# Kernel optimization log

Hardware: AMD Instinct MI355X
Metric: run time of the kernel (lower is better)

## Reference

```python
import jax, jax.numpy as jnp
import numpy as np
import math

B, S, D, H = 2, 2048, 1024, 16
DK = D // H


def setup_inputs() -> dict:
    key = jax.random.key(0)
    ks = jax.random.split(key, 12)
    scale = 1.0 / math.sqrt(D)
    inp = {
        "q": jax.random.normal(ks[0], (B, S, D), jnp.float32),
        "k": jax.random.normal(ks[1], (B, S, D), jnp.float32),
        "v": jax.random.normal(ks[2], (B, S, D), jnp.float32),
        # causal mask, broadcast over batch and heads; 0 entries are masked out
        "mask": jnp.tril(jnp.ones((S, S), jnp.int32))[None, None, :, :],
        "wq_w": jax.random.normal(ks[3], (D, D), jnp.float32) * scale,
        "wq_b": jax.random.normal(ks[4], (D,), jnp.float32) * 0.01,
        "wk_w": jax.random.normal(ks[5], (D, D), jnp.float32) * scale,
        "wk_b": jax.random.normal(ks[6], (D,), jnp.float32) * 0.01,
        "wv_w": jax.random.normal(ks[7], (D, D), jnp.float32) * scale,
        "wv_b": jax.random.normal(ks[8], (D,), jnp.float32) * 0.01,
        "wo_w": jax.random.normal(ks[9], (D, D), jnp.float32) * scale,
        "wo_b": jax.random.normal(ks[10], (D,), jnp.float32) * 0.01,
    }
    return inp


def _mha(q, k, v, mask, wq_w, wq_b, wk_w, wk_b, wv_w, wv_b, wo_w, wo_b):
    # nn.Linear: x @ W^T + b
    def split_heads(x):  # [B,S,D] -> [B,H,S,DK]
        return x.reshape(B, S, H, DK).transpose(0, 2, 1, 3)

    Q = split_heads(q @ wq_w.T + wq_b)
    K = split_heads(k @ wk_w.T + wk_b)
    V = split_heads(v @ wv_w.T + wv_b)

    scores = jnp.einsum("bhqd,bhkd->bhqk", Q, K) / math.sqrt(DK)  # [B,H,S,S]
    scores = jnp.where(mask == 0, jnp.float32(-1e9), scores)
    # NOTE: source uses softmax(dim=1) == over the HEADS axis; replicated faithfully.
    attn = jax.nn.softmax(scores, axis=1)
    out = jnp.einsum("bhqk,bhkd->bhqd", attn, V)  # [B,H,S,DK]
    out = out.transpose(0, 2, 1, 3).reshape(B, S, D)
    return out @ wo_w.T + wo_b


def reference(q, k, v, mask, wq_w, wq_b, wk_w, wk_b, wv_w, wv_b, wo_w, wo_b):
    return _mha(q, k, v, mask, wq_w, wq_b, wk_w, wk_b, wv_w, wv_b, wo_w, wo_b)
```

## Files before the change

kernel.cpp:

```cpp
#include <hip/hip_runtime.h>
#include <hip/hip_bf16.h>
#include <stdint.h>


#define BB 2
#define SS 2048
#define DD 1024
#define HH 16
#define DKK 64

typedef __attribute__((ext_vector_type(8))) short bf16x8;
typedef __attribute__((ext_vector_type(4))) float f32x4;

typedef __attribute__((address_space(3))) uint32_t lds32_t;
typedef __attribute__((address_space(1))) uint32_t g32_t;

__device__ __forceinline__ void async_cp16(void* lds, const void* g){
    __builtin_amdgcn_global_load_lds((const g32_t*)g, (lds32_t*)lds, 16, 0, 0);
}

__device__ __forceinline__ float bf_lo(uint32_t w){ return __uint_as_float(w << 16); }
__device__ __forceinline__ float bf_hi(uint32_t w){ return __uint_as_float(w & 0xffff0000u); }
__device__ __forceinline__ uint16_t f2bf(float f){
    uint32_t x = __float_as_uint(f);
    return (uint16_t)((x + 0x7fffu + ((x >> 16) & 1u)) >> 16);
}
__device__ __forceinline__ void u4tof8(uint4 u, float* f){
    f[0]=bf_lo(u.x); f[1]=bf_hi(u.x);
    f[2]=bf_lo(u.y); f[3]=bf_hi(u.y);
    f[4]=bf_lo(u.z); f[5]=bf_hi(u.z);
    f[6]=bf_lo(u.w); f[7]=bf_hi(u.w);
}
__device__ __forceinline__ uint4 pack8u(const float* f){
    uint4 r;
    r.x = (uint32_t)f2bf(f[0]) | ((uint32_t)f2bf(f[1]) << 16);
    r.y = (uint32_t)f2bf(f[2]) | ((uint32_t)f2bf(f[3]) << 16);
    r.z = (uint32_t)f2bf(f[4]) | ((uint32_t)f2bf(f[5]) << 16);
    r.w = (uint32_t)f2bf(f[6]) | ((uint32_t)f2bf(f[7]) << 16);
    return r;
}

__global__ __launch_bounds__(256) void cvt_all(
    const float* __restrict__ w0, const float* __restrict__ w1,
    const float* __restrict__ w2, const float* __restrict__ w3,
    const float* __restrict__ a0, const float* __restrict__ a1,
    const float* __restrict__ a2,
    uint16_t* __restrict__ dw0, uint16_t* __restrict__ dw1,
    uint16_t* __restrict__ dw2, uint16_t* __restrict__ dw3,
    uint16_t* __restrict__ da0, uint16_t* __restrict__ da1,
    uint16_t* __restrict__ da2)
{
    const int y = blockIdx.y;
    const float* s; uint16_t* d; int n4;
    switch (y) {
        case 0: s = w0; d = dw0; n4 = 262144; break;
        case 1: s = w1; d = dw1; n4 = 262144; break;
        case 2: s = w2; d = dw2; n4 = 262144; break;
        case 3: s = w3; d = dw3; n4 = 262144; break;
        case 4: s = a0; d = da0; n4 = 1048576; break;
        case 5: s = a1; d = da1; n4 = 1048576; break;
        default: s = a2; d = da2; n4 = 1048576; break;
    }
    int i = blockIdx.x * 256 + threadIdx.x;
    if (i >= n4) return;
    float4 v = ((const float4*)s)[i];
    uint32_t lo = (uint32_t)f2bf(v.x) | ((uint32_t)f2bf(v.y) << 16);
    uint32_t hi = (uint32_t)f2bf(v.z) | ((uint32_t)f2bf(v.w) << 16);
    ((uint2*)d)[i] = make_uint2(lo, hi);
}

template <int OMODE>
__global__ __launch_bounds__(256) void gemm_bt(
    const uint16_t* __restrict__ A, const uint16_t* __restrict__ W,
    const float* __restrict__ bias, void* __restrict__ Cout)
{
    __shared__ uint16_t As[128][32];
    __shared__ uint16_t Bs[128][32];

    const int t    = threadIdx.x;
    const int bm   = blockIdx.x * 128;
    const int bn   = blockIdx.y * 128;
    const int lane = t & 63;
    const int w    = t >> 6;
    const int wm   = (w >> 1) * 64;
    const int wn   = (w & 1) * 64;
    const int lm   = lane & 15;
    const int quad = lane >> 4;

    f32x4 acc[4][4] = {};

    const int lr = lane >> 2;
    const int lc = (lane & 3) * 8;

    for (int k0 = 0; k0 < DD; k0 += 32) {
#pragma unroll
        for (int i2 = 0; i2 < 2; ++i2) {
            const int i = w * 2 + i2;
            async_cp16(&As[16*i][0], &A[(size_t)(bm + 16*i + lr) * DD + k0 + lc]);
            async_cp16(&Bs[16*i][0], &W[(size_t)(bn + 16*i + lr) * DD + k0 + lc]);
        }
        __syncthreads();
        bf16x8 af[4], bf[4];
#pragma unroll
        for (int mt = 0; mt < 4; ++mt) af[mt] = *(const bf16x8*)&As[wm + 16*mt + lm][quad*8];
#pragma unroll
        for (int nt = 0; nt < 4; ++nt) bf[nt] = *(const bf16x8*)&Bs[wn + 16*nt + lm][quad*8];
#pragma unroll
        for (int mt = 0; mt < 4; ++mt)
#pragma unroll
            for (int nt = 0; nt < 4; ++nt)
                acc[mt][nt] = __builtin_amdgcn_mfma_f32_16x16x32_bf16(af[mt], bf[nt], acc[mt][nt], 0, 0, 0);
        __syncthreads();
    }

#pragma unroll
    for (int nt = 0; nt < 4; ++nt) {
        const int ng = bn + wn + 16*nt + lm;
        const float bv = bias[ng];
#pragma unroll
        for (int mt = 0; mt < 4; ++mt) {
            const int m0 = bm + wm + 16*mt + quad*4;
            if (OMODE == 1) {
                const int bb = m0 >> 11, s0 = m0 & (SS - 1);
                const int hh = ng >> 6,  dk = ng & 63;
                float v0 = acc[mt][nt][0] + bv, v1 = acc[mt][nt][1] + bv;
                float v2 = acc[mt][nt][2] + bv, v3 = acc[mt][nt][3] + bv;
                uint2 wv;
                wv.x = (uint32_t)f2bf(v0) | ((uint32_t)f2bf(v1) << 16);
                wv.y = (uint32_t)f2bf(v2) | ((uint32_t)f2bf(v3) << 16);
                *(uint2*)&((uint16_t*)Cout)[(((size_t)(bb*HH + hh))*DKK + dk)*SS + s0] = wv;
            } else {
#pragma unroll
                for (int r = 0; r < 4; ++r) {
                    const int m = m0 + r;
                    const float val = acc[mt][nt][r] + bv;
                    if (OMODE == 0) {
                        const int bb = m >> 11, s = m & (SS - 1);
                        const int hh = ng >> 6, dk = ng & 63;
                        ((uint16_t*)Cout)[(((size_t)(bb*HH + hh))*SS + s)*DKK + dk] = f2bf(val);
                    } else {
                        ((float*)Cout)[(size_t)m * DD + ng] = val;
                    }
                }
            }
        }
    }
}

__global__ __launch_bounds__(256) void suf_kernel(
    const uint16_t* __restrict__ Vt, float* __restrict__ Suf)
{
    const int bh = blockIdx.x;
    const int t  = threadIdx.x;
    const int d = t & 63, seg = t >> 6;
    __shared__ float cs[64][65];
    const uint16_t* row = Vt + ((size_t)bh * DKK + d) * SS;
    for (int cl = 0; cl < 16; ++cl) {
        const int c = seg * 16 + cl;
        float sum = 0.f;
#pragma unroll
        for (int j = 0; j < 4; ++j) {
            uint4 u = *(const uint4*)&row[c * 32 + j * 8];
            float f[8]; u4tof8(u, f);
            sum += ((f[0]+f[1])+(f[2]+f[3])) + ((f[4]+f[5])+(f[6]+f[7]));
        }
        cs[c][d] = sum;
    }
    __syncthreads();
    if (t < 64) {
        float run = 0.f;
        Suf[((size_t)bh * 65 + 64) * DKK + t] = 0.f;
        for (int c = 63; c >= 0; --c) {
            run += cs[c][t];
            Suf[((size_t)bh * 65 + c) * DKK + t] = run;
        }
    }
}

__global__ __launch_bounds__(1024) void attn_v4(
    const uint16_t* __restrict__ Qc, const uint16_t* __restrict__ Kc,
    const uint16_t* __restrict__ Vt, const float* __restrict__ Suf,
    uint16_t* __restrict__ AOp)
{
    __shared__ uint16_t E[2][16][32][40];
    __shared__ uint16_t Zr[32][40];

    const int x  = blockIdx.x;
    const int p  = x & 3;
    const int b  = (x >> 2) & 1;
    const int pr = x >> 3;
    const int tid  = threadIdx.x;
    const int h    = tid >> 6;
    const int lane = tid & 63;
    const int lm   = lane & 15;
    const int quad = lane >> 4;

    const uint16_t* Qh = Qc + ((size_t)(b*HH + h)) * SS * DKK;
    const uint16_t* Kh = Kc + ((size_t)(b*HH + h)) * SS * DKK;
    const uint16_t* Vh = Vt + ((size_t)(b*HH + h)) * DKK * SS;
    uint16_t* AOb = AOp + ((size_t)(p*BB + b)) * SS * DD;

    const int rq = tid >> 4;
    const int rk2 = tid & 15;

    int cc = 0;
#pragma unroll
    for (int tt = 0; tt < 2; ++tt) {
        const int tq = tt ? (63 - pr) : pr;
        const int q0 = tq * 32;

        bf16x8 qf[2][2];
#pragma unroll
        for (int qt = 0; qt < 2; ++qt)
#pragma unroll
            for (int kd = 0; kd < 2; ++kd)
                qf[qt][kd] = *(const bf16x8*)&Qh[(size_t)(q0 + 16*qt + lm)*DKK + kd*32 + quad*8];

        f32x4 oacc[2][4] = {};

        for (int c = p; c <= tq; c += 4, ++cc) {
            const int buf = cc & 1;
            const int k0 = c * 32;
            bf16x8 vf[4];
#pragma unroll
            for (int dt = 0; dt < 4; ++dt)
                vf[dt] = *(const bf16x8*)&Vh[(size_t)(16*dt + lm)*SS + k0 + quad*8];
            f32x4 sacc[2][2] = {};
#pragma unroll
            for (int kt = 0; kt < 2; ++kt) {
                bf16x8 kf0 = *(const bf16x8*)&Kh[(size_t)(k0 + 16*kt + lm)*DKK + quad*8];
                bf16x8 kf1 = *(const bf16x8*)&Kh[(size_t)(k0 + 16*kt + lm)*DKK + 32 + quad*8];
#pragma unroll
                for (int qt = 0; qt < 2; ++qt) {
                    sacc[kt][qt] = __builtin_amdgcn_mfma_f32_16x16x32_bf16(kf0, qf[qt][0], sacc[kt][qt], 0, 0, 0);
                    sacc[kt][qt] = __builtin_amdgcn_mfma_f32_16x16x32_bf16(kf1, qf[qt][1], sacc[kt][qt], 0, 0, 0);
                }
            }
#pragma unroll
            for (int kt = 0; kt < 2; ++kt)
#pragma unroll
                for (int qt = 0; qt < 2; ++qt) {
                    const int qg = q0 + 16*qt + lm;
                    uint16_t ev[4];
#pragma unroll
                    for (int r = 0; r < 4; ++r) {
                        const int kg = k0 + 16*kt + quad*4 + r;
                        ev[r] = f2bf((kg > qg) ? 1.0f : __expf(sacc[kt][qt][r] * 0.125f));
                    }
                    uint2 evw;
                    evw.x = (uint32_t)ev[0] | ((uint32_t)ev[1] << 16);
                    evw.y = (uint32_t)ev[2] | ((uint32_t)ev[3] << 16);
                    *(uint2*)&E[buf][h][16*qt + lm][16*kt + quad*4] = evw;
                }
            __syncthreads();
            if (tid < 512) {
                float z0 = 0.f, z1 = 0.f;
#pragma unroll
                for (int i = 0; i < 16; ++i) {
                    uint32_t wv2 = *(const uint32_t*)&E[buf][i][rq][rk2*2];
                    z0 += bf_lo(wv2); z1 += bf_hi(wv2);
                }
                *(uint32_t*)&Zr[rq][rk2*2] =
                    (uint32_t)f2bf(__fdividef(1.f, z0)) | ((uint32_t)f2bf(__fdividef(1.f, z1)) << 16);
            }
            __syncthreads();
#pragma unroll
            for (int qt = 0; qt < 2; ++qt) {
                uint4 eu = *(const uint4*)&E[buf][h][16*qt + lm][quad*8];
                uint4 zu = *(const uint4*)&Zr[16*qt + lm][quad*8];
                float ef[8], zf[8];
                u4tof8(eu, ef); u4tof8(zu, zf);
                float pf[8];
#pragma unroll
                for (int j = 0; j < 8; ++j) pf[j] = ef[j] * zf[j];
                uint4 pu = pack8u(pf);
                bf16x8 pa = *(bf16x8*)&pu;
#pragma unroll
                for (int dt = 0; dt < 4; ++dt)
                    oacc[qt][dt] = __builtin_amdgcn_mfma_f32_16x16x32_bf16(pa, vf[dt], oacc[qt][dt], 0, 0, 0);
            }
        }

        float corr[4] = {0.f, 0.f, 0.f, 0.f};
        if (p == 0) {
            const float* Sf = Suf + ((size_t)(b*HH + h) * 65 + (tq + 1)) * DKK;
#pragma unroll
            for (int dt = 0; dt < 4; ++dt) corr[dt] = 0.0625f * Sf[16*dt + lm];
        }
#pragma unroll
        for (int qt = 0; qt < 2; ++qt)
#pragma unroll
            for (int dt = 0; dt < 4; ++dt)
#pragma unroll
                for (int r = 0; r < 4; ++r) {
                    const int s = q0 + 16*qt + quad*4 + r;
                    AOb[(size_t)s * DD + h*DKK + 16*dt + lm] = f2bf(oacc[qt][dt][r] + corr[dt]);
                }
    }
}

__global__ __launch_bounds__(256) void reduce4(uint16_t* AOp)
{
    const size_t P1 = (size_t)BB * SS * DD;
    const int i = blockIdx.x * 256 + threadIdx.x;
    uint2 u0 = ((const uint2*)AOp)[i];
    uint2 u1 = ((const uint2*)(AOp + P1))[i];
    uint2 u2 = ((const uint2*)(AOp + 2*P1))[i];
    uint2 u3 = ((const uint2*)(AOp + 3*P1))[i];
    float r[4];
    r[0] = (bf_lo(u0.x) + bf_lo(u1.x)) + (bf_lo(u2.x) + bf_lo(u3.x));
    r[1] = (bf_hi(u0.x) + bf_hi(u1.x)) + (bf_hi(u2.x) + bf_hi(u3.x));
    r[2] = (bf_lo(u0.y) + bf_lo(u1.y)) + (bf_lo(u2.y) + bf_lo(u3.y));
    r[3] = (bf_hi(u0.y) + bf_hi(u1.y)) + (bf_hi(u2.y) + bf_hi(u3.y));
    uint2 wv;
    wv.x = (uint32_t)f2bf(r[0]) | ((uint32_t)f2bf(r[1]) << 16);
    wv.y = (uint32_t)f2bf(r[2]) | ((uint32_t)f2bf(r[3]) << 16);
    ((uint2*)AOp)[i] = wv;
}

extern "C" void kernel_launch(void* const* d_in, const int* in_sizes, int n_in,
                              void* d_out, int out_size, void* d_ws, size_t ws_size,
                              hipStream_t stream)
{
    const float* q    = (const float*)d_in[0];
    const float* k    = (const float*)d_in[1];
    const float* v    = (const float*)d_in[2];
    const float* wq_w = (const float*)d_in[4];
    const float* wq_b = (const float*)d_in[5];
    const float* wk_w = (const float*)d_in[6];
    const float* wk_b = (const float*)d_in[7];
    const float* wv_w = (const float*)d_in[8];
    const float* wv_b = (const float*)d_in[9];
    const float* wo_w = (const float*)d_in[10];
    const float* wo_b = (const float*)d_in[11];
    float* out = (float*)d_out;

    uint16_t* wsu = (uint16_t*)d_ws;
    const size_t M1 = (size_t)1 << 20;
    uint16_t* wcq = wsu + 0 * M1;
    uint16_t* wck = wsu + 1 * M1;
    uint16_t* wcv = wsu + 2 * M1;
    uint16_t* wco = wsu + 3 * M1;
    uint16_t* Qc  = wsu + 4 * M1;
    uint16_t* Kc  = wsu + 8 * M1;
    uint16_t* Vt  = wsu + 12 * M1;
    uint16_t* AOp = wsu + 16 * M1;
    uint16_t* xq  = wsu + 16 * M1;
    uint16_t* xk  = wsu + 20 * M1;
    uint16_t* xv  = wsu + 24 * M1;
    float*    Suf = (float*)wcq;

    cvt_all<<<dim3(4096, 7), 256, 0, stream>>>(
        wq_w, wk_w, wv_w, wo_w, q, k, v,
        wcq, wck, wcv, wco, xq, xk, xv);

    dim3 ggrid(32, 8);
    gemm_bt<0><<<ggrid, 256, 0, stream>>>(xq, wcq, wq_b, Qc);
    gemm_bt<0><<<ggrid, 256, 0, stream>>>(xk, wck, wk_b, Kc);
    gemm_bt<1><<<ggrid, 256, 0, stream>>>(xv, wcv, wv_b, Vt);

    suf_kernel<<<32, 256, 0, stream>>>(Vt, Suf);
    attn_v4<<<256, 1024, 0, stream>>>(Qc, Kc, Vt, Suf, AOp);

    reduce4<<<4096, 256, 0, stream>>>(AOp);
    gemm_bt<2><<<ggrid, 256, 0, stream>>>(AOp, wco, wo_b, out);
}
```

Baseline: 316.5 us.

## Switch to fp16 with packed math, merge QKV GEMMs, split attention blocks per query tile

All intermediate storage moves from bf16 to fp16, using packed RTZ converts and packed half multiplies in place of the manual bf16 rounding and unpacking. The three projection GEMMs become one launch with a z-dimension of three. The attention kernel now handles a single query tile per block over 512 blocks instead of two tiles over 256, and drops the double-buffered E array, which adds a barrier before each E write. The aim is to cut conversion ALU work and launch overhead and to expose more parallelism, at the cost of fp16 range and rounding risk and more imbalanced block lengths.

```diff
diff --git a/kernel.cpp b/kernel.cpp
--- a/kernel.cpp
+++ b/kernel.cpp
@@ -1,5 +1,4 @@
 #include <hip/hip_runtime.h>
-#include <hip/hip_bf16.h>
 #include <stdint.h>
 
 
@@ -9,7 +8,10 @@
 #define HH 16
 #define DKK 64
 
-typedef __attribute__((ext_vector_type(8))) short bf16x8;
+typedef _Float16 f16;
+typedef __attribute__((ext_vector_type(2))) _Float16 f16x2;
+typedef __attribute__((ext_vector_type(8))) _Float16 f16x8;
+typedef __attribute__((ext_vector_type(2))) __fp16 fp16x2_raw;
 typedef __attribute__((ext_vector_type(4))) float f32x4;
 
 typedef __attribute__((address_space(3))) uint32_t lds32_t;
@@ -19,25 +21,18 @@
     __builtin_amdgcn_global_load_lds((const g32_t*)g, (lds32_t*)lds, 16, 0, 0);
 }
 
-__device__ __forceinline__ float bf_lo(uint32_t w){ return __uint_as_float(w << 16); }
-__device__ __forceinline__ float bf_hi(uint32_t w){ return __uint_as_float(w & 0xffff0000u); }
-__device__ __forceinline__ uint16_t f2bf(float f){
-    uint32_t x = __float_as_uint(f);
-    return (uint16_t)((x + 0x7fffu + ((x >> 16) & 1u)) >> 16);
-}
-__device__ __forceinline__ void u4tof8(uint4 u, float* f){
-    f[0]=bf_lo(u.x); f[1]=bf_hi(u.x);
-    f[2]=bf_lo(u.y); f[3]=bf_hi(u.y);
-    f[4]=bf_lo(u.z); f[5]=bf_hi(u.z);
-    f[6]=bf_lo(u.w); f[7]=bf_hi(u.w);
-}
-__device__ __forceinline__ uint4 pack8u(const float* f){
-    uint4 r;
-    r.x = (uint32_t)f2bf(f[0]) | ((uint32_t)f2bf(f[1]) << 16);
-    r.y = (uint32_t)f2bf(f[2]) | ((uint32_t)f2bf(f[3]) << 16);
-    r.z = (uint32_t)f2bf(f[4]) | ((uint32_t)f2bf(f[5]) << 16);
-    r.w = (uint32_t)f2bf(f[6]) | ((uint32_t)f2bf(f[7]) << 16);
-    return r;
+union U32H { uint32_t u; f16x2 h; fp16x2_raw hr; };
+
+__device__ __forceinline__ uint32_t pk2(float a, float b){
+    U32H c; c.hr = __builtin_amdgcn_cvt_pkrtz(a, b); return c.u;
+}
+__device__ __forceinline__ float h_lo(uint32_t w){ U32H c; c.u = w; return (float)c.h[0]; }
+__device__ __forceinline__ float h_hi(uint32_t w){ U32H c; c.u = w; return (float)c.h[1]; }
+__device__ __forceinline__ uint32_t pkmul(uint32_t a, uint32_t b){
+    U32H x, y, r; x.u = a; y.u = b; r.h = x.h * y.h; return r.u;
+}
+__device__ __forceinline__ uint16_t f2h(float f){
+    union { f16 h; uint16_t u; } c; c.h = (f16)f; return c.u;
 }
 
 __global__ __launch_bounds__(256) void cvt_all(
@@ -64,19 +59,15 @@
     int i = blockIdx.x * 256 + threadIdx.x;
     if (i >= n4) return;
     float4 v = ((const float4*)s)[i];
-    uint32_t lo = (uint32_t)f2bf(v.x) | ((uint32_t)f2bf(v.y) << 16);
-    uint32_t hi = (uint32_t)f2bf(v.z) | ((uint32_t)f2bf(v.w) << 16);
-    ((uint2*)d)[i] = make_uint2(lo, hi);
+    ((uint2*)d)[i] = make_uint2(pk2(v.x, v.y), pk2(v.z, v.w));
 }
 
 template <int OMODE>
-__global__ __launch_bounds__(256) void gemm_bt(
+__device__ __forceinline__ void gemm_core(
+    uint16_t (*As)[32], uint16_t (*Bs)[32],
     const uint16_t* __restrict__ A, const uint16_t* __restrict__ W,
     const float* __restrict__ bias, void* __restrict__ Cout)
 {
-    __shared__ uint16_t As[128][32];
-    __shared__ uint16_t Bs[128][32];
-
     const int t    = threadIdx.x;
     const int bm   = blockIdx.x * 128;
     const int bn   = blockIdx.y * 128;
@@ -100,16 +91,16 @@
             async_cp16(&Bs[16*i][0], &W[(size_t)(bn + 16*i + lr) * DD + k0 + lc]);
         }
         __syncthreads();
-        bf16x8 af[4], bf[4];
-#pragma unroll
-        for (int mt = 0; mt < 4; ++mt) af[mt] = *(const bf16x8*)&As[wm + 16*mt + lm][quad*8];
-#pragma unroll
-        for (int nt = 0; nt < 4; ++nt) bf[nt] = *(const bf16x8*)&Bs[wn + 16*nt + lm][quad*8];
+        f16x8 a8[4], b8[4];
+#pragma unroll
+        for (int mt = 0; mt < 4; ++mt) a8[mt] = *(const f16x8*)&As[wm + 16*mt + lm][quad*8];
+#pragma unroll
+        for (int nt = 0; nt < 4; ++nt) b8[nt] = *(const f16x8*)&Bs[wn + 16*nt + lm][quad*8];
 #pragma unroll
         for (int mt = 0; mt < 4; ++mt)
 #pragma unroll
             for (int nt = 0; nt < 4; ++nt)
-                acc[mt][nt] = __builtin_amdgcn_mfma_f32_16x16x32_bf16(af[mt], bf[nt], acc[mt][nt], 0, 0, 0);
+                acc[mt][nt] = __builtin_amdgcn_mfma_f32_16x16x32_f16(a8[mt], b8[nt], acc[mt][nt], 0, 0, 0);
         __syncthreads();
     }
 
@@ -123,11 +114,9 @@
             if (OMODE == 1) {
                 const int bb = m0 >> 11, s0 = m0 & (SS - 1);
                 const int hh = ng >> 6,  dk = ng & 63;
-                float v0 = acc[mt][nt][0] + bv, v1 = acc[mt][nt][1] + bv;
-                float v2 = acc[mt][nt][2] + bv, v3 = acc[mt][nt][3] + bv;
                 uint2 wv;
-                wv.x = (uint32_t)f2bf(v0) | ((uint32_t)f2bf(v1) << 16);
-                wv.y = (uint32_t)f2bf(v2) | ((uint32_t)f2bf(v3) << 16);
+                wv.x = pk2(acc[mt][nt][0] + bv, acc[mt][nt][1] + bv);
+                wv.y = pk2(acc[mt][nt][2] + bv, acc[mt][nt][3] + bv);
                 *(uint2*)&((uint16_t*)Cout)[(((size_t)(bb*HH + hh))*DKK + dk)*SS + s0] = wv;
             } else {
 #pragma unroll
@@ -137,7 +126,7 @@
                     if (OMODE == 0) {
                         const int bb = m >> 11, s = m & (SS - 1);
                         const int hh = ng >> 6, dk = ng & 63;
-                        ((uint16_t*)Cout)[(((size_t)(bb*HH + hh))*SS + s)*DKK + dk] = f2bf(val);
+                        ((uint16_t*)Cout)[(((size_t)(bb*HH + hh))*SS + s)*DKK + dk] = f2h(val);
                     } else {
                         ((float*)Cout)[(size_t)m * DD + ng] = val;
                     }
@@ -145,6 +134,31 @@
             }
         }
     }
+}
+
+__global__ __launch_bounds__(256) void gemm_qkv(
+    const uint16_t* __restrict__ xq, const uint16_t* __restrict__ wq,
+    const float* __restrict__ bq, uint16_t* __restrict__ Qc,
+    const uint16_t* __restrict__ xk, const uint16_t* __restrict__ wk,
+    const float* __restrict__ bk, uint16_t* __restrict__ Kc,
+    const uint16_t* __restrict__ xv, const uint16_t* __restrict__ wv,
+    const float* __restrict__ bv, uint16_t* __restrict__ Vt)
+{
+    __shared__ __align__(16) uint16_t As[128][32];
+    __shared__ __align__(16) uint16_t Bs[128][32];
+    const int z = blockIdx.z;
+    if (z == 0)      gemm_core<0>(As, Bs, xq, wq, bq, Qc);
+    else if (z == 1) gemm_core<0>(As, Bs, xk, wk, bk, Kc);
+    else             gemm_core<1>(As, Bs, xv, wv, bv, Vt);
+}
+
+__global__ __launch_bounds__(256) void gemm_o(
+    const uint16_t* __restrict__ A, const uint16_t* __restrict__ W,
+    const float* __restrict__ bias, float* __restrict__ Cout)
+{
+    __shared__ __align__(16) uint16_t As[128][32];
+    __shared__ __align__(16) uint16_t Bs[128][32];
+    gemm_core<2>(As, Bs, A, W, bias, Cout);
 }
 
 __global__ __launch_bounds__(256) void suf_kernel(
@@ -159,10 +173,10 @@
         const int c = seg * 16 + cl;
         float sum = 0.f;
 #pragma unroll
-        for (int j = 0; j < 4; ++j) {
-            uint4 u = *(const uint4*)&row[c * 32 + j * 8];
-            float f[8]; u4tof8(u, f);
-            sum += ((f[0]+f[1])+(f[2]+f[3])) + ((f[4]+f[5])+(f[6]+f[7]));
+        for (int jj = 0; jj < 4; ++jj) {
+            uint4 u = *(const uint4*)&row[c * 32 + jj * 8];
+            sum += ((h_lo(u.x)+h_hi(u.x)) + (h_lo(u.y)+h_hi(u.y)))
+                 + ((h_lo(u.z)+h_hi(u.z)) + (h_lo(u.w)+h_hi(u.w)));
         }
         cs[c][d] = sum;
     }
@@ -177,18 +191,19 @@
     }
 }
 
-__global__ __launch_bounds__(1024) void attn_v4(
+__global__ __launch_bounds__(1024, 8) void attn_v5(
     const uint16_t* __restrict__ Qc, const uint16_t* __restrict__ Kc,
     const uint16_t* __restrict__ Vt, const float* __restrict__ Suf,
     uint16_t* __restrict__ AOp)
 {
-    __shared__ uint16_t E[2][16][32][40];
-    __shared__ uint16_t Zr[32][40];
+    __shared__ __align__(16) uint16_t E[16][32][40];
+    __shared__ __align__(16) uint16_t Zr[32][40];
 
     const int x  = blockIdx.x;
     const int p  = x & 3;
     const int b  = (x >> 2) & 1;
-    const int pr = x >> 3;
+    const int j  = x >> 3;
+    const int tq = (j < 32) ? j : 95 - j;
     const int tid  = threadIdx.x;
     const int h    = tid >> 6;
     const int lane = tid & 63;
@@ -200,103 +215,91 @@
     const uint16_t* Vh = Vt + ((size_t)(b*HH + h)) * DKK * SS;
     uint16_t* AOb = AOp + ((size_t)(p*BB + b)) * SS * DD;
 
-    const int rq = tid >> 4;
+    const int rq  = tid >> 4;
     const int rk2 = tid & 15;
 
-    int cc = 0;
-#pragma unroll
-    for (int tt = 0; tt < 2; ++tt) {
-        const int tq = tt ? (63 - pr) : pr;
-        const int q0 = tq * 32;
-
-        bf16x8 qf[2][2];
-#pragma unroll
-        for (int qt = 0; qt < 2; ++qt)
-#pragma unroll
-            for (int kd = 0; kd < 2; ++kd)
-                qf[qt][kd] = *(const bf16x8*)&Qh[(size_t)(q0 + 16*qt + lm)*DKK + kd*32 + quad*8];
-
-        f32x4 oacc[2][4] = {};
-
-        for (int c = p; c <= tq; c += 4, ++cc) {
-            const int buf = cc & 1;
-            const int k0 = c * 32;
-            bf16x8 vf[4];
+    const int q0 = tq * 32;
+
+    f16x8 qf[2][2];
+#pragma unroll
+    for (int qt = 0; qt < 2; ++qt)
+#pragma unroll
+        for (int kd = 0; kd < 2; ++kd)
+            qf[qt][kd] = *(const f16x8*)&Qh[(size_t)(q0 + 16*qt + lm)*DKK + kd*32 + quad*8];
+
+    f32x4 oacc[2][4] = {};
+
+    for (int c = p; c <= tq; c += 4) {
+        const int k0 = c * 32;
+        f16x8 vf[4];
+#pragma unroll
+        for (int dt = 0; dt < 4; ++dt)
+            vf[dt] = *(const f16x8*)&Vh[(size_t)(16*dt + lm)*SS + k0 + quad*8];
+        f32x4 sacc[2][2] = {};
+#pragma unroll
+        for (int kt = 0; kt < 2; ++kt) {
+            f16x8 kf0 = *(const f16x8*)&Kh[(size_t)(k0 + 16*kt + lm)*DKK + quad*8];
+            f16x8 kf1 = *(const f16x8*)&Kh[(size_t)(k0 + 16*kt + lm)*DKK + 32 + quad*8];
+#pragma unroll
+            for (int qt = 0; qt < 2; ++qt) {
+                sacc[kt][qt] = __builtin_amdgcn_mfma_f32_16x16x32_f16(kf0, qf[qt][0], sacc[kt][qt], 0, 0, 0);
+                sacc[kt][qt] = __builtin_amdgcn_mfma_f32_16x16x32_f16(kf1, qf[qt][1], sacc[kt][qt], 0, 0, 0);
+            }
+        }
+        __syncthreads();
+#pragma unroll
+        for (int kt = 0; kt < 2; ++kt)
+#pragma unroll
+            for (int qt = 0; qt < 2; ++qt) {
+                const int qg = q0 + 16*qt + lm;
+                float e[4];
+#pragma unroll
+                for (int r = 0; r < 4; ++r) {
+                    const int kg = k0 + 16*kt + quad*4 + r;
+                    e[r] = (kg > qg) ? 1.0f : __expf(sacc[kt][qt][r] * 0.125f);
+                }
+                uint2 evw = make_uint2(pk2(e[0], e[1]), pk2(e[2], e[3]));
+                *(uint2*)&E[h][16*qt + lm][16*kt + quad*4] = evw;
+            }
+        __syncthreads();
+        if (tid < 512) {
+            float z0 = 0.f, z1 = 0.f;
+#pragma unroll
+            for (int i = 0; i < 16; ++i) {
+                uint32_t wv2 = *(const uint32_t*)&E[i][rq][rk2*2];
+                z0 += h_lo(wv2); z1 += h_hi(wv2);
+            }
+            *(uint32_t*)&Zr[rq][rk2*2] = pk2(__fdividef(1.f, z0), __fdividef(1.f, z1));
+        }
+        __syncthreads();
+#pragma unroll
+        for (int qt = 0; qt < 2; ++qt) {
+            uint4 eu = *(const uint4*)&E[h][16*qt + lm][quad*8];
+            uint4 zu = *(const uint4*)&Zr[16*qt + lm][quad*8];
+            union { uint4 u; f16x8 v; } P;
+            P.u.x = pkmul(eu.x, zu.x); P.u.y = pkmul(eu.y, zu.y);
+            P.u.z = pkmul(eu.z, zu.z); P.u.w = pkmul(eu.w, zu.w);
 #pragma unroll
             for (int dt = 0; dt < 4; ++dt)
-                vf[dt] = *(const bf16x8*)&Vh[(size_t)(16*dt + lm)*SS + k0 + quad*8];
-            f32x4 sacc[2][2] = {};
-#pragma unroll
-            for (int kt = 0; kt < 2; ++kt) {
-                bf16x8 kf0 = *(const bf16x8*)&Kh[(size_t)(k0 + 16*kt + lm)*DKK + quad*8];
-                bf16x8 kf1 = *(const bf16x8*)&Kh[(size_t)(k0 + 16*kt + lm)*DKK + 32 + quad*8];
-#pragma unroll
-                for (int qt = 0; qt < 2; ++qt) {
-                    sacc[kt][qt] = __builtin_amdgcn_mfma_f32_16x16x32_bf16(kf0, qf[qt][0], sacc[kt][qt], 0, 0, 0);
-                    sacc[kt][qt] = __builtin_amdgcn_mfma_f32_16x16x32_bf16(kf1, qf[qt][1], sacc[kt][qt], 0, 0, 0);
-                }
-            }
-#pragma unroll
-            for (int kt = 0; kt < 2; ++kt)
-#pragma unroll
-                for (int qt = 0; qt < 2; ++qt) {
-                    const int qg = q0 + 16*qt + lm;
-                    uint16_t ev[4];
-#pragma unroll
-                    for (int r = 0; r < 4; ++r) {
-                        const int kg = k0 + 16*kt + quad*4 + r;
-                        ev[r] = f2bf((kg > qg) ? 1.0f : __expf(sacc[kt][qt][r] * 0.125f));
-                    }
-                    uint2 evw;
-                    evw.x = (uint32_t)ev[0] | ((uint32_t)ev[1] << 16);
-                    evw.y = (uint32_t)ev[2] | ((uint32_t)ev[3] << 16);
-                    *(uint2*)&E[buf][h][16*qt + lm][16*kt + quad*4] = evw;
-                }
-            __syncthreads();
-            if (tid < 512) {
-                float z0 = 0.f, z1 = 0.f;
-#pragma unroll
-                for (int i = 0; i < 16; ++i) {
-                    uint32_t wv2 = *(const uint32_t*)&E[buf][i][rq][rk2*2];
-                    z0 += bf_lo(wv2); z1 += bf_hi(wv2);
-                }
-                *(uint32_t*)&Zr[rq][rk2*2] =
-                    (uint32_t)f2bf(__fdividef(1.f, z0)) | ((uint32_t)f2bf(__fdividef(1.f, z1)) << 16);
-            }
-            __syncthreads();
-#pragma unroll
-            for (int qt = 0; qt < 2; ++qt) {
-                uint4 eu = *(const uint4*)&E[buf][h][16*qt + lm][quad*8];
-                uint4 zu = *(const uint4*)&Zr[16*qt + lm][quad*8];
-                float ef[8], zf[8];
-                u4tof8(eu, ef); u4tof8(zu, zf);
-                float pf[8];
-#pragma unroll
-                for (int j = 0; j < 8; ++j) pf[j] = ef[j] * zf[j];
-                uint4 pu = pack8u(pf);
-                bf16x8 pa = *(bf16x8*)&pu;
-#pragma unroll
-                for (int dt = 0; dt < 4; ++dt)
-                    oacc[qt][dt] = __builtin_amdgcn_mfma_f32_16x16x32_bf16(pa, vf[dt], oacc[qt][dt], 0, 0, 0);
-            }
-        }
-
-        float corr[4] = {0.f, 0.f, 0.f, 0.f};
-        if (p == 0) {
-            const float* Sf = Suf + ((size_t)(b*HH + h) * 65 + (tq + 1)) * DKK;
-#pragma unroll
-            for (int dt = 0; dt < 4; ++dt) corr[dt] = 0.0625f * Sf[16*dt + lm];
-        }
-#pragma unroll
-        for (int qt = 0; qt < 2; ++qt)
-#pragma unroll
-            for (int dt = 0; dt < 4; ++dt)
-#pragma unroll
-                for (int r = 0; r < 4; ++r) {
-                    const int s = q0 + 16*qt + quad*4 + r;
-                    AOb[(size_t)s * DD + h*DKK + 16*dt + lm] = f2bf(oacc[qt][dt][r] + corr[dt]);
-                }
-    }
+                oacc[qt][dt] = __builtin_amdgcn_mfma_f32_16x16x32_f16(P.v, vf[dt], oacc[qt][dt], 0, 0, 0);
+        }
+    }
+
+    float corr[4] = {0.f, 0.f, 0.f, 0.f};
+    if (p == 0) {
+        const float* Sf = Suf + ((size_t)(b*HH + h) * 65 + (tq + 1)) * DKK;
+#pragma unroll
+        for (int dt = 0; dt < 4; ++dt) corr[dt] = 0.0625f * Sf[16*dt + lm];
+    }
+#pragma unroll
+    for (int qt = 0; qt < 2; ++qt)
+#pragma unroll
+        for (int dt = 0; dt < 4; ++dt)
+#pragma unroll
+            for (int r = 0; r < 4; ++r) {
+                const int s = q0 + 16*qt + quad*4 + r;
+                AOb[(size_t)s * DD + h*DKK + 16*dt + lm] = f2h(oacc[qt][dt][r] + corr[dt]);
+            }
 }
 
 __global__ __launch_bounds__(256) void reduce4(uint16_t* AOp)
@@ -307,15 +310,11 @@
     uint2 u1 = ((const uint2*)(AOp + P1))[i];
     uint2 u2 = ((const uint2*)(AOp + 2*P1))[i];
     uint2 u3 = ((const uint2*)(AOp + 3*P1))[i];
-    float r[4];
-    r[0] = (bf_lo(u0.x) + bf_lo(u1.x)) + (bf_lo(u2.x) + bf_lo(u3.x));
-    r[1] = (bf_hi(u0.x) + bf_hi(u1.x)) + (bf_hi(u2.x) + bf_hi(u3.x));
-    r[2] = (bf_lo(u0.y) + bf_lo(u1.y)) + (bf_lo(u2.y) + bf_lo(u3.y));
-    r[3] = (bf_hi(u0.y) + bf_hi(u1.y)) + (bf_hi(u2.y) + bf_hi(u3.y));
-    uint2 wv;
-    wv.x = (uint32_t)f2bf(r[0]) | ((uint32_t)f2bf(r[1]) << 16);
-    wv.y = (uint32_t)f2bf(r[2]) | ((uint32_t)f2bf(r[3]) << 16);
-    ((uint2*)AOp)[i] = wv;
+    float r0 = (h_lo(u0.x) + h_lo(u1.x)) + (h_lo(u2.x) + h_lo(u3.x));
+    float r1 = (h_hi(u0.x) + h_hi(u1.x)) + (h_hi(u2.x) + h_hi(u3.x));
+    float r2 = (h_lo(u0.y) + h_lo(u1.y)) + (h_lo(u2.y) + h_lo(u3.y));
+    float r3 = (h_hi(u0.y) + h_hi(u1.y)) + (h_hi(u2.y) + h_hi(u3.y));
+    ((uint2*)AOp)[i] = make_uint2(pk2(r0, r1), pk2(r2, r3));
 }
 
 extern "C" void kernel_launch(void* const* d_in, const int* in_sizes, int n_in,
@@ -354,14 +353,14 @@
         wq_w, wk_w, wv_w, wo_w, q, k, v,
         wcq, wck, wcv, wco, xq, xk, xv);
 
-    dim3 ggrid(32, 8);
-    gemm_bt<0><<<ggrid, 256, 0, stream>>>(xq, wcq, wq_b, Qc);
-    gemm_bt<0><<<ggrid, 256, 0, stream>>>(xk, wck, wk_b, Kc);
-    gemm_bt<1><<<ggrid, 256, 0, stream>>>(xv, wcv, wv_b, Vt);
+    gemm_qkv<<<dim3(32, 8, 3), 256, 0, stream>>>(
+        xq, wcq, wq_b, Qc,
+        xk, wck, wk_b, Kc,
+        xv, wcv, wv_b, Vt);
 
     suf_kernel<<<32, 256, 0, stream>>>(Vt, Suf);
-    attn_v4<<<256, 1024, 0, stream>>>(Qc, Kc, Vt, Suf, AOp);
+    attn_v5<<<512, 1024, 0, stream>>>(Qc, Kc, Vt, Suf, AOp);
 
     reduce4<<<4096, 256, 0, stream>>>(AOp);
-    gemm_bt<2><<<ggrid, 256, 0, stream>>>(AOp, wco, wo_b, out);
-}
+    gemm_o<<<dim3(32, 8), 256, 0, stream>>>(AOp, wco, wo_b, out);
+}
```

Measured after the change: 473.0 us. 49.4% more time.
